# Performance work log

Measured on AMD Instinct MI355X. Metric: run time of the kernel, lower is better.

Reference implementation:

```python
import jax, jax.numpy as jnp
import numpy as np

DIM = 128

def setup_inputs() -> dict:
    key = jax.random.key(0)
    ks = jax.random.split(key, 4)
    N, C, L = 64, DIM, 4096
    scale = 1.0 / np.sqrt(DIM)
    return {
        "x": jax.random.normal(ks[0], (N, C, L), dtype=jnp.float32),
        "Wq": jax.random.normal(ks[1], (DIM, DIM), dtype=jnp.float32) * scale,
        "bq": jnp.zeros((DIM,), dtype=jnp.float32),
        "Wk": jax.random.normal(ks[2], (DIM, DIM), dtype=jnp.float32) * scale,
        "bk": jnp.zeros((DIM,), dtype=jnp.float32),
        "Wv": jax.random.normal(ks[3], (DIM, DIM), dtype=jnp.float32) * scale,
        "bv": jnp.zeros((DIM,), dtype=jnp.float32),
    }

def reference(x, Wq, bq, Wk, bk, Wv, bv):
    # x: [N, C, L] -> rearrange to [N, L, C]
    h = jnp.transpose(x, (0, 2, 1))                       # [N, L, C]
    q = jnp.einsum('nlc,cd->nld', h, Wq) + bq             # [N, L, D]
    k = jnp.einsum('nlc,cd->nld', h, Wk) + bk             # [N, L, D]
    v = jnp.einsum('nlc,cd->nld', h, Wv) + bv             # [N, L, D]
    # AFT-Simple: softmax over sequence axis of K, global weighted pool of V
    w = jax.nn.softmax(k, axis=1)                         # [N, L, D]
    pooled = jnp.sum(w * v, axis=1, keepdims=True)        # [N, 1, D]
    out = jax.nn.sigmoid(q) * pooled                      # [N, L, D]
    return jnp.transpose(out, (0, 2, 1))                  # [N, C, L]
```

## Files before the change

### kernel.cpp

```cpp
#include <hip/hip_runtime.h>
#include <hip/hip_bf16.h>

#define NB 64
#define CD 128
#define LL 4096
#define LCHUNK 64
#define NCHUNK 64

typedef __attribute__((ext_vector_type(8))) short short8;
typedef __attribute__((ext_vector_type(4))) float f32x4;

#define LOG2E 1.4426950408889634f

#define WT_OFF   0
#define WSS_OFF  (1u<<20)
#define WSP_OFF  ((1u<<20) + NB*NCHUNK*CD*4)
#define POOL_OFF ((1u<<20) + 2u*NB*NCHUNK*CD*4)

__device__ __forceinline__ unsigned short f2bf(float f) {
    union { float f; unsigned u; } v; v.f = f;
    unsigned r = v.u + 0x7FFFu + ((v.u >> 16) & 1u);
    return (unsigned short)(r >> 16);
}
__device__ __forceinline__ unsigned pack2(float lo, float hi) {
    union { __hip_bfloat162 h; unsigned u; } v;
    v.h = __float22bfloat162_rn(float2{lo, hi});
    return v.u;
}

__global__ void prep_wt(const float* __restrict__ Wq, const float* __restrict__ Wk,
                        const float* __restrict__ Wv, unsigned short* __restrict__ wt) {
    int t = blockIdx.x >> 7;
    int d = blockIdx.x & 127;
    const float* W = (t == 0) ? Wq : (t == 1) ? Wk : Wv;
    int c = threadIdx.x;
    wt[((size_t)t*CD + d)*CD + c] = f2bf(W[c*CD + d]);
}

__device__ __forceinline__ void stage_x(const float* __restrict__ x, char* lds_x,
                                        int n, int l0, int tid) {
    const int f = tid & 15, tg = tid >> 4;
#pragma unroll
    for (int it = 0; it < 4; ++it) {
        int cp = tg + 16*it;
        f32x4 lo = *(const f32x4*)(x + ((size_t)n*CD + 2*cp    )*LL + l0 + 4*f);
        f32x4 hi = *(const f32x4*)(x + ((size_t)n*CD + 2*cp + 1)*LL + l0 + 4*f);
        char* base = lds_x + (4*f)*272 + 16*((cp >> 2) ^ (f & 7)) + 4*(cp & 3);
#pragma unroll
        for (int j = 0; j < 4; ++j)
            *(unsigned*)(base + j*272) = pack2(lo[j], hi[j]);
    }
}

__global__ __launch_bounds__(256, 4)
void aft_kv(const float* __restrict__ x, const unsigned short* __restrict__ wt,
            const float* __restrict__ bk, const float* __restrict__ bv,
            float* __restrict__ wsS, float* __restrict__ wsP) {
    __shared__ char lds_x[64 * 272];
    const int tid = threadIdx.x;
    const int n = blockIdx.x >> 6;
    const int ch = blockIdx.x & 63;
    const int l0 = ch * LCHUNK;
    const int w = tid >> 6, lane = tid & 63, r = lane & 15, g = lane >> 4;

    short8 b_k[2][4], b_v[2][4];
    float bkl[2], bvl[2];
#pragma unroll
    for (int dt = 0; dt < 2; ++dt) {
        int d = 32*w + 16*dt + r;
#pragma unroll
        for (int s = 0; s < 4; ++s) {
            b_k[dt][s] = *(const short8*)(wt + ((size_t)(1*CD + d))*CD + 32*s + 8*g);
            b_v[dt][s] = *(const short8*)(wt + ((size_t)(2*CD + d))*CD + 32*s + 8*g);
        }
        bkl[dt] = bk[d];
        bvl[dt] = bv[d];
    }

    stage_x(x, lds_x, n, l0, tid);
    __syncthreads();

    float s_run[2] = {0.f, 0.f}, p_run[2] = {0.f, 0.f};

#pragma unroll
    for (int lt = 0; lt < 4; ++lt) {
        const int lrow = 16*lt + r;
        const int lsw = (lrow >> 2) & 7;
        short8 a[4];
#pragma unroll
        for (int s = 0; s < 4; ++s)
            a[s] = *(const short8*)(lds_x + lrow*272 + 16*((4*s + g) ^ lsw));
        f32x4 ak[2], av[2];
#pragma unroll
        for (int dt = 0; dt < 2; ++dt) { ak[dt] = (f32x4){0,0,0,0}; av[dt] = (f32x4){0,0,0,0}; }
#pragma unroll
        for (int s = 0; s < 4; ++s) {
            ak[0] = __builtin_amdgcn_mfma_f32_16x16x32_bf16(a[s], b_k[0][s], ak[0], 0,0,0);
            ak[1] = __builtin_amdgcn_mfma_f32_16x16x32_bf16(a[s], b_k[1][s], ak[1], 0,0,0);
            av[0] = __builtin_amdgcn_mfma_f32_16x16x32_bf16(a[s], b_v[0][s], av[0], 0,0,0);
            av[1] = __builtin_amdgcn_mfma_f32_16x16x32_bf16(a[s], b_v[1][s], av[1], 0,0,0);
        }
#pragma unroll
        for (int dt = 0; dt < 2; ++dt)
#pragma unroll
            for (int v = 0; v < 4; ++v) {
                float e = __builtin_amdgcn_exp2f((ak[dt][v] + bkl[dt]) * LOG2E);
                s_run[dt] += e;
                p_run[dt] += e * (av[dt][v] + bvl[dt]);
            }
    }

#pragma unroll
    for (int dt = 0; dt < 2; ++dt) {
        float s = s_run[dt], p = p_run[dt];
        s += __shfl_xor(s, 16, 64);  p += __shfl_xor(p, 16, 64);
        s += __shfl_xor(s, 32, 64);  p += __shfl_xor(p, 32, 64);
        if (g == 0) {
            size_t idx = ((size_t)n*NCHUNK + ch)*CD + 32*w + 16*dt + r;
            wsS[idx] = s;
            wsP[idx] = p;
        }
    }
}

__global__ void aft_pass2(const float* __restrict__ wsS, const float* __restrict__ wsP,
                          float* __restrict__ pooled) {
    int n = blockIdx.x, d = threadIdx.x;
    float s = 0.f, p = 0.f;
    for (int b = 0; b < NCHUNK; ++b) {
        size_t idx = ((size_t)n*NCHUNK + b)*CD + d;
        s += wsS[idx];
        p += wsP[idx];
    }
    pooled[(size_t)n*CD + d] = p / s;
}

__global__ __launch_bounds__(256, 4)
void aft_q(const float* __restrict__ x, const unsigned short* __restrict__ wt,
           const float* __restrict__ bq, const float* __restrict__ pooled,
           float* __restrict__ out) {
    __shared__ char lds_x[64 * 272];
    const int tid = threadIdx.x;
    const int n = blockIdx.x >> 6;
    const int ch = blockIdx.x & 63;
    const int l0 = ch * LCHUNK;
    const int w = tid >> 6, lane = tid & 63, r = lane & 15, g = lane >> 4;

    short8 b_q[2][4];
    float bql[2], pll[2];
#pragma unroll
    for (int dt = 0; dt < 2; ++dt) {
        int d = 32*w + 16*dt + r;
#pragma unroll
        for (int s = 0; s < 4; ++s)
            b_q[dt][s] = *(const short8*)(wt + ((size_t)(0*CD + d))*CD + 32*s + 8*g);
        bql[dt] = bq[d];
        pll[dt] = pooled[(size_t)n*CD + d];
    }

    stage_x(x, lds_x, n, l0, tid);
    __syncthreads();

#pragma unroll
    for (int lt = 0; lt < 4; ++lt) {
        const int lrow = 16*lt + r;
        const int lsw = (lrow >> 2) & 7;
        short8 a[4];
#pragma unroll
        for (int s = 0; s < 4; ++s)
            a[s] = *(const short8*)(lds_x + lrow*272 + 16*((4*s + g) ^ lsw));
        f32x4 aq[2];
        aq[0] = (f32x4){0,0,0,0};
        aq[1] = (f32x4){0,0,0,0};
#pragma unroll
        for (int s = 0; s < 4; ++s) {
            aq[0] = __builtin_amdgcn_mfma_f32_16x16x32_bf16(a[s], b_q[0][s], aq[0], 0,0,0);
            aq[1] = __builtin_amdgcn_mfma_f32_16x16x32_bf16(a[s], b_q[1][s], aq[1], 0,0,0);
        }
#pragma unroll
        for (int dt = 0; dt < 2; ++dt) {
            f32x4 o;
#pragma unroll
            for (int v = 0; v < 4; ++v) {
                float q2 = (aq[dt][v] + bql[dt]) * LOG2E;
                o[v] = pll[dt] * __builtin_amdgcn_rcpf(1.f + __builtin_amdgcn_exp2f(-q2));
            }
            *(f32x4*)(out + ((size_t)n*CD + 32*w + 16*dt + r)*LL + l0 + 16*lt + 4*g) = o;
        }
    }
}

extern "C" void kernel_launch(void* const* d_in, const int* in_sizes, int n_in,
                              void* d_out, int out_size, void* d_ws, size_t ws_size,
                              hipStream_t stream) {
    const float* x  = (const float*)d_in[0];
    const float* Wq = (const float*)d_in[1];
    const float* bq = (const float*)d_in[2];
    const float* Wk = (const float*)d_in[3];
    const float* bk = (const float*)d_in[4];
    const float* Wv = (const float*)d_in[5];
    const float* bv = (const float*)d_in[6];
    float* out = (float*)d_out;
    char* ws = (char*)d_ws;
    unsigned short* wt = (unsigned short*)(ws + WT_OFF);
    float* wsS = (float*)(ws + WSS_OFF);
    float* wsP = (float*)(ws + WSP_OFF);
    float* pooled = (float*)(ws + POOL_OFF);

    prep_wt<<<384, 128, 0, stream>>>(Wq, Wk, Wv, wt);
    aft_kv<<<NB * NCHUNK, 256, 0, stream>>>(x, wt, bk, bv, wsS, wsP);
    aft_pass2<<<NB, CD, 0, stream>>>(wsS, wsP, pooled);
    aft_q<<<NB * NCHUNK, 256, 0, stream>>>(x, wt, bq, pooled, out);
}
```

Before: 101.6 us.

## Fuse Q projection into KV pass and store bf16 sigmoid gate for a scale pass

The Q projection and sigmoid now run inside the K/V kernel, so x is read from memory only once. The gate sigmoid(q) is written to a bf16 workspace. A new lightweight elementwise kernel multiplies that workspace by the pooled vector and writes the fp32 output. This removes the second read of x and its re-staging, at the cost of writing and re-reading a 64MB bf16 intermediate and rounding the gate to bf16 before the final multiply. The x staging is also moved ahead of the weight loads to overlap the two.

```diff
diff --git a/kernel.cpp b/kernel.cpp
--- a/kernel.cpp
+++ b/kernel.cpp
@@ -9,6 +9,7 @@
 
 typedef __attribute__((ext_vector_type(8))) short short8;
 typedef __attribute__((ext_vector_type(4))) float f32x4;
+typedef __attribute__((ext_vector_type(2))) unsigned u32x2;
 
 #define LOG2E 1.4426950408889634f
 
@@ -16,11 +17,16 @@
 #define WSS_OFF  (1u<<20)
 #define WSP_OFF  ((1u<<20) + NB*NCHUNK*CD*4)
 #define POOL_OFF ((1u<<20) + 2u*NB*NCHUNK*CD*4)
+#define WSQ_OFF  (8u<<20)
 
 __device__ __forceinline__ unsigned short f2bf(float f) {
     union { float f; unsigned u; } v; v.f = f;
     unsigned r = v.u + 0x7FFFu + ((v.u >> 16) & 1u);
     return (unsigned short)(r >> 16);
+}
+__device__ __forceinline__ float bf2f(unsigned short h) {
+    union { unsigned u; float f; } v; v.u = ((unsigned)h) << 16;
+    return v.f;
 }
 __device__ __forceinline__ unsigned pack2(float lo, float hi) {
     union { __hip_bfloat162 h; unsigned u; } v;
@@ -53,9 +59,11 @@
 }
 
 __global__ __launch_bounds__(256, 4)
-void aft_kv(const float* __restrict__ x, const unsigned short* __restrict__ wt,
-            const float* __restrict__ bk, const float* __restrict__ bv,
-            float* __restrict__ wsS, float* __restrict__ wsP) {
+void aft_qkv(const float* __restrict__ x, const unsigned short* __restrict__ wt,
+             const float* __restrict__ bq, const float* __restrict__ bk,
+             const float* __restrict__ bv,
+             float* __restrict__ wsS, float* __restrict__ wsP,
+             unsigned short* __restrict__ wsq) {
     __shared__ char lds_x[64 * 272];
     const int tid = threadIdx.x;
     const int n = blockIdx.x >> 6;
@@ -63,6 +71,8 @@
     const int l0 = ch * LCHUNK;
     const int w = tid >> 6, lane = tid & 63, r = lane & 15, g = lane >> 4;
 
+    stage_x(x, lds_x, n, l0, tid);
+
     short8 b_k[2][4], b_v[2][4];
     float bkl[2], bvl[2];
 #pragma unroll
@@ -77,7 +87,6 @@
         bvl[dt] = bv[d];
     }
 
-    stage_x(x, lds_x, n, l0, tid);
     __syncthreads();
 
     float s_run[2] = {0.f, 0.f}, p_run[2] = {0.f, 0.f};
@@ -108,6 +117,17 @@
                 s_run[dt] += e;
                 p_run[dt] += e * (av[dt][v] + bvl[dt]);
             }
+    }
+
+    short8 b_q[2][4];
+    float bql[2];
+#pragma unroll
+    for (int dt = 0; dt < 2; ++dt) {
+        int d = 32*w + 16*dt + r;
+#pragma unroll
+        for (int s = 0; s < 4; ++s)
+            b_q[dt][s] = *(const short8*)(wt + ((size_t)(0*CD + d))*CD + 32*s + 8*g);
+        bql[dt] = bq[d];
     }
 
 #pragma unroll
@@ -121,6 +141,35 @@
             wsP[idx] = p;
         }
     }
+
+#pragma unroll
+    for (int lt = 0; lt < 4; ++lt) {
+        const int lrow = 16*lt + r;
+        const int lsw = (lrow >> 2) & 7;
+        short8 a[4];
+#pragma unroll
+        for (int s = 0; s < 4; ++s)
+            a[s] = *(const short8*)(lds_x + lrow*272 + 16*((4*s + g) ^ lsw));
+        f32x4 aq[2];
+        aq[0] = (f32x4){0,0,0,0};
+        aq[1] = (f32x4){0,0,0,0};
+#pragma unroll
+        for (int s = 0; s < 4; ++s) {
+            aq[0] = __builtin_amdgcn_mfma_f32_16x16x32_bf16(a[s], b_q[0][s], aq[0], 0,0,0);
+            aq[1] = __builtin_amdgcn_mfma_f32_16x16x32_bf16(a[s], b_q[1][s], aq[1], 0,0,0);
+        }
+#pragma unroll
+        for (int dt = 0; dt < 2; ++dt) {
+            float sg[4];
+#pragma unroll
+            for (int v = 0; v < 4; ++v) {
+                float q2 = (aq[dt][v] + bql[dt]) * LOG2E;
+                sg[v] = __builtin_amdgcn_rcpf(1.f + __builtin_amdgcn_exp2f(-q2));
+            }
+            u32x2 val = { pack2(sg[0], sg[1]), pack2(sg[2], sg[3]) };
+            *(u32x2*)(wsq + ((size_t)n*CD + 32*w + 16*dt + r)*LL + l0 + 16*lt + 4*g) = val;
+        }
+    }
 }
 
 __global__ void aft_pass2(const float* __restrict__ wsS, const float* __restrict__ wsP,
@@ -135,59 +184,24 @@
     pooled[(size_t)n*CD + d] = p / s;
 }
 
-__global__ __launch_bounds__(256, 4)
-void aft_q(const float* __restrict__ x, const unsigned short* __restrict__ wt,
-           const float* __restrict__ bq, const float* __restrict__ pooled,
-           float* __restrict__ out) {
-    __shared__ char lds_x[64 * 272];
-    const int tid = threadIdx.x;
-    const int n = blockIdx.x >> 6;
-    const int ch = blockIdx.x & 63;
-    const int l0 = ch * LCHUNK;
-    const int w = tid >> 6, lane = tid & 63, r = lane & 15, g = lane >> 4;
-
-    short8 b_q[2][4];
-    float bql[2], pll[2];
-#pragma unroll
-    for (int dt = 0; dt < 2; ++dt) {
-        int d = 32*w + 16*dt + r;
-#pragma unroll
-        for (int s = 0; s < 4; ++s)
-            b_q[dt][s] = *(const short8*)(wt + ((size_t)(0*CD + d))*CD + 32*s + 8*g);
-        bql[dt] = bq[d];
-        pll[dt] = pooled[(size_t)n*CD + d];
-    }
-
-    stage_x(x, lds_x, n, l0, tid);
-    __syncthreads();
-
-#pragma unroll
-    for (int lt = 0; lt < 4; ++lt) {
-        const int lrow = 16*lt + r;
-        const int lsw = (lrow >> 2) & 7;
-        short8 a[4];
-#pragma unroll
-        for (int s = 0; s < 4; ++s)
-            a[s] = *(const short8*)(lds_x + lrow*272 + 16*((4*s + g) ^ lsw));
-        f32x4 aq[2];
-        aq[0] = (f32x4){0,0,0,0};
-        aq[1] = (f32x4){0,0,0,0};
-#pragma unroll
-        for (int s = 0; s < 4; ++s) {
-            aq[0] = __builtin_amdgcn_mfma_f32_16x16x32_bf16(a[s], b_q[0][s], aq[0], 0,0,0);
-            aq[1] = __builtin_amdgcn_mfma_f32_16x16x32_bf16(a[s], b_q[1][s], aq[1], 0,0,0);
-        }
-#pragma unroll
-        for (int dt = 0; dt < 2; ++dt) {
-            f32x4 o;
-#pragma unroll
-            for (int v = 0; v < 4; ++v) {
-                float q2 = (aq[dt][v] + bql[dt]) * LOG2E;
-                o[v] = pll[dt] * __builtin_amdgcn_rcpf(1.f + __builtin_amdgcn_exp2f(-q2));
-            }
-            *(f32x4*)(out + ((size_t)n*CD + 32*w + 16*dt + r)*LL + l0 + 16*lt + 4*g) = o;
-        }
-    }
+__global__ __launch_bounds__(256)
+void aft_pass3(const unsigned short* __restrict__ wsq, const float* __restrict__ pooled,
+               float* __restrict__ out) {
+    const int b = blockIdx.x;
+    const int n = b >> 8;
+    const int d = (b >> 1) & 127;
+    const int half = b & 1;
+    const float pl = pooled[(size_t)n*CD + d];
+    const size_t base = ((size_t)n*CD + d)*LL + half*2048 + threadIdx.x*8;
+    short8 v = *(const short8*)(wsq + base);
+    f32x4 o0, o1;
+#pragma unroll
+    for (int j = 0; j < 4; ++j) {
+        o0[j] = bf2f((unsigned short)v[j]) * pl;
+        o1[j] = bf2f((unsigned short)v[4+j]) * pl;
+    }
+    *(f32x4*)(out + base) = o0;
+    *(f32x4*)(out + base + 4) = o1;
 }
 
 extern "C" void kernel_launch(void* const* d_in, const int* in_sizes, int n_in,
@@ -206,9 +220,10 @@
     float* wsS = (float*)(ws + WSS_OFF);
     float* wsP = (float*)(ws + WSP_OFF);
     float* pooled = (float*)(ws + POOL_OFF);
+    unsigned short* wsq = (unsigned short*)(ws + WSQ_OFF);
 
     prep_wt<<<384, 128, 0, stream>>>(Wq, Wk, Wv, wt);
-    aft_kv<<<NB * NCHUNK, 256, 0, stream>>>(x, wt, bk, bv, wsS, wsP);
+    aft_qkv<<<NB * NCHUNK, 256, 0, stream>>>(x, wt, bq, bk, bv, wsS, wsP, wsq);
     aft_pass2<<<NB, CD, 0, stream>>>(wsS, wsP, pooled);
-    aft_q<<<NB * NCHUNK, 256, 0, stream>>>(x, wt, bq, pooled, out);
-}
+    aft_pass3<<<NB * CD * 2, 256, 0, stream>>>(wsq, pooled, out);
+}
```

Measured after the change: 140.3 us. 38.1% more time.
